# Kernel optimization log

Measured on AMD Instinct MI355X. Metric: run time of the kernel, lower is better.

## Reference

```python
import jax, jax.numpy as jnp
import numpy as np

WS = 8           # window_size
NH = 8           # num_heads
VD = 384         # values_dim
CD = 128         # coords_dim
ID = 384         # inner_dim = inner_ratio * values_dim
HD = ID // NH    # head_dim = 48


def _rel_bias(pos_emb):
    # static Swin relative-position index table, gathers from pos_emb [2*WS-1, 2*WS-1]
    idx = np.array([[x, y] for x in range(WS) for y in range(WS)])
    rel = idx[None, :, :] - idx[:, None, :] + WS - 1  # [64,64,2]
    return pos_emb[rel[:, :, 0], rel[:, :, 1]]        # [64,64]


def _rmsnorm(x, w, eps=1e-6):
    return x * jax.lax.rsqrt(jnp.mean(x * x, axis=-1, keepdims=True) + eps) * w


def _to_windows(t):
    # t: [b, Hp, Wp, D] with feature layout (e H) -> [b, NH, Wh, Ww, WS*WS, e]
    b, Hp, Wp, D = t.shape
    e = D // NH
    t = t.reshape(b, Hp // WS, WS, Wp // WS, WS, e, NH)
    t = t.transpose(0, 6, 1, 3, 2, 4, 5)
    return t.reshape(b, NH, Hp // WS, Wp // WS, WS * WS, e)


def setup_inputs() -> dict:
    key = jax.random.key(0)
    ks = jax.random.split(key, 8)
    B, H, W = 2, 192, 192
    s = 0.02
    return {
        "values": jax.random.normal(ks[0], (B, H, W, VD), jnp.float32),
        "coords": jax.random.normal(ks[1], (B, H, W, CD), jnp.float32),
        "W_vqk": jax.random.normal(ks[2], (VD, 2 * ID), jnp.float32) * s,
        "b_vqk": jnp.zeros((2 * ID,), jnp.float32),
        "g_vqk": jnp.ones((2 * ID,), jnp.float32),
        "W_vv": jax.random.normal(ks[3], (VD, ID), jnp.float32) * s,
        "b_vv": jnp.zeros((ID,), jnp.float32),
        "W_cqk": jax.random.normal(ks[4], (CD, 2 * ID), jnp.float32) * s,
        "b_cqk": jnp.zeros((2 * ID,), jnp.float32),
        "g_cqk": jnp.ones((2 * ID,), jnp.float32),
        "att_lambda": jax.random.normal(ks[5], (1,), jnp.float32),
        "pos_emb": jax.random.normal(ks[6], (2 * WS - 1, 2 * WS - 1), jnp.float32),
        "W_ov": jax.random.normal(ks[7], (ID, VD), jnp.float32) * s,
        "b_ov": jnp.zeros((VD,), jnp.float32),
    }


def reference(values, coords, W_vqk, b_vqk, g_vqk, W_vv, b_vv,
              W_cqk, b_cqk, g_cqk, att_lambda, pos_emb, W_ov, b_ov):
    b, h, w, _ = values.shape  # h, w divisible by WS -> torch F.pad would add 0
    # values path: cat([RMSNorm(Linear_qk(x)), Linear_v(x)]); '(d k)' with k=3
    # means q/k/v are INTERLEAVED along the feature dim (index d*3+k).
    vqk = _rmsnorm(values @ W_vqk + b_vqk, g_vqk)            # [b,h,w,2*ID]
    vv_ = values @ W_vv + b_vv                               # [b,h,w,ID]
    vcat = jnp.concatenate([vqk, vv_], axis=-1).reshape(b, h, w, ID, 3)
    qv, kv, vv = vcat[..., 0], vcat[..., 1], vcat[..., 2]
    # coords path (update_coords=False): interleaved split k=2
    cqk = _rmsnorm(coords @ W_cqk + b_cqk, g_cqk).reshape(b, h, w, ID, 2)
    qc, kc = cqk[..., 0], cqk[..., 1]
    # shifted=True: roll by -WS//2 (NOTE: original never rolls back)
    shift = -(WS // 2)
    roll = lambda t: jnp.roll(t, (shift, shift), axis=(1, 2))
    qv, kv, vv, qc, kc = (_to_windows(roll(t)) for t in (qv, kv, vv, qc, kc))
    # fused value+coord scores with learned lambda
    dots = (jnp.einsum('bHxyie,bHxyje->bHxyij', qv, kv)
            + att_lambda[0] * jnp.einsum('bHxyie,bHxyje->bHxyij', qc, kc)) / np.sqrt(HD)
    dots = dots + _rel_bias(pos_emb)
    # shifted-window masks on last window row / last window column
    s = WS * (WS // 2)
    n = WS * WS
    row_mask = jnp.zeros((n, n), jnp.float32)
    row_mask = row_mask.at[-s:, :-s].set(-jnp.inf).at[:-s, -s:].set(-jnp.inf)
    col_mask = row_mask.reshape(WS, WS, WS, WS).transpose(1, 0, 3, 2).reshape(n, n)
    dots = dots.at[:, :, -1, :].add(row_mask)
    dots = dots.at[:, :, :, -1].add(col_mask)
    att = jax.nn.softmax(dots, axis=-1)
    yv = jnp.einsum('bHxyij,bHxyje->bHxyie', att, vv)  # [b,NH,Wh,Ww,64,HD]
    Wh, Ww = h // WS, w // WS
    # output layout '(H e)' -> heads slow, e fast
    yv = yv.reshape(b, NH, Wh, Ww, WS, WS, HD).transpose(0, 2, 4, 3, 5, 1, 6)
    yv = yv.reshape(b, Wh * WS, Ww * WS, ID)[:, :h, :w, :]
    return yv @ W_ov + b_ov
```

## Files before the change

### kernel.cpp

```cpp
#include <hip/hip_runtime.h>
#include <hip/hip_bf16.h>

typedef __hip_bfloat16 bf16;
typedef __attribute__((ext_vector_type(8))) short bf16x8;
typedef __attribute__((ext_vector_type(4))) float f32x4;

#define CPIX 12288

__device__ __forceinline__ float tof(bf16 x){ return __bfloat162float(x); }
__device__ __forceinline__ bf16  tob(float x){ return __float2bfloat16(x); }
__device__ __forceinline__ float bf2f(short s){ return __uint_as_float(((unsigned)(unsigned short)s) << 16); }

__global__ __launch_bounds__(256) void wprep_k(
    const float* __restrict__ W_vqk, const float* __restrict__ W_vv, const float* __restrict__ W_cqk,
    const float* __restrict__ W_ov,  const float* __restrict__ b_vqk, const float* __restrict__ b_vv,
    const float* __restrict__ b_cqk, const float* __restrict__ g_vqk, const float* __restrict__ g_cqk,
    bf16* __restrict__ W1Tp, bf16* __restrict__ WcTp, bf16* __restrict__ WoT,
    float* __restrict__ bP0, float* __restrict__ bPc, float* __restrict__ gvP, float* __restrict__ gcP,
    float* __restrict__ rs_v, float* __restrict__ rs_c)
{
  int idx = blockIdx.x*256 + threadIdx.x;
  if (idx < 442368) {
    int n = idx/384, k = idx - n*384;
    int role = n/384, rem = n - role*384, h = rem/48, e = rem - (rem/48)*48;
    int c = 24*e + 3*h + role;
    float v = (e < 32) ? W_vqk[k*768 + c] : W_vv[k*384 + (c - 768)];
    W1Tp[n*384 + k] = tob(v);
  } else if (idx < 540672) {
    int q = idx - 442368;
    int n = q >> 7, k = q & 127;
    int role = n/384, rem = n - role*384, h = rem/48, e = rem - (rem/48)*48;
    WcTp[n*128 + k] = tob(W_cqk[k*768 + 16*e + 2*h + role]);
  } else if (idx < 688128) {
    int q = idx - 540672;
    int n = q/384, k = q - n*384;
    WoT[n*384 + k] = tob(W_ov[k*384 + n]);
  } else if (idx < 689280) {
    int n = idx - 688128;
    int role = n/384, rem = n - role*384, h = rem/48, e = rem - (rem/48)*48;
    int c = 24*e + 3*h + role;
    bP0[n] = (e < 32) ? b_vqk[c] : b_vv[c - 768];
  } else if (idx < 690048) {
    int n = idx - 689280;
    int role = n/384, rem = n - role*384, h = rem/48, e = rem - (rem/48)*48;
    bPc[n] = b_cqk[16*e + 2*h + role];
  } else if (idx < 691200) {
    int n = idx - 690048;
    int role = n/384, rem = n - role*384, h = rem/48, e = rem - (rem/48)*48;
    gvP[n] = (e < 32) ? g_vqk[24*e + 3*h + role] : 1.0f;
  } else if (idx < 691968) {
    int n = idx - 691200;
    int role = n/384, rem = n - role*384, h = rem/48, e = rem - (rem/48)*48;
    gcP[n] = g_cqk[16*e + 2*h + role];
  } else if (idx < 716544) {
    int q = idx - 691968;
    if (q < CPIX) rs_v[q] = 0.f; else rs_c[q - CPIX] = 0.f;
  }
}

template<int MODE>
__global__ __launch_bounds__(256,4) void gemm_k(const float* __restrict__ Af, const bf16* __restrict__ Ab,
    const bf16* __restrict__ WT, const float* __restrict__ biasP,
    bf16* __restrict__ outb, float* __restrict__ outf, float* __restrict__ rsum,
    float* __restrict__ z0, float* __restrict__ z1, int bb, int hf, int pix0)
{
  constexpr int KTOT = (MODE==1) ? 128 : 384;
  constexpr int NT   = (MODE==0) ? 1152 : (MODE==1) ? 768 : 384;
  constexpr int BM   = (MODE==2) ? 64 : 128;
  constexpr int MT4  = BM/32;
  constexpr int ACH  = BM*8;
  __shared__ bf16 As[BM][72];
  __shared__ bf16 Bs[128][72];
  const int tid = threadIdx.x, lane = tid & 63, wid = tid >> 6;
  const int wr = (wid >> 1)*(BM/2), wc = (wid & 1)*64;
  const int rowbase = blockIdx.x*BM;
  const int nbase   = blockIdx.y*128;

  if constexpr (MODE == 2) {
    if (blockIdx.y == 0) {
      if (tid < 64) z0[rowbase + tid] = 0.f;
      else if (tid < 128) z1[rowbase + tid - 64] = 0.f;
    }
  }

  f32x4 acc[MT4][4] = {};
  for (int ks = 0; ks < KTOT; ks += 64) {
    __syncthreads();
    #pragma unroll
    for (int it = 0; it < (ACH + 1024)/256; it++) {
      int idx = it*256 + tid;
      if (idx < ACH) {
        int r = idx >> 3, c = idx & 7;
        if constexpr (MODE == 2) {
          *(uint4*)&As[r][c*8] = *(const uint4*)(Ab + (size_t)(rowbase + r)*KTOT + ks + c*8);
        } else {
          int pix = rowbase + r;
          int lr = pix/192, lc = pix - (pix/192)*192;
          int srow = (hf*64 + lr + 4) % 192;
          int scol = (lc + 4) % 192;
          const float* src = Af + (((size_t)bb*192 + srow)*192 + scol)*KTOT + ks + c*8;
          float4 f0 = *(const float4*)src;
          float4 f1 = *(const float4*)(src + 4);
          union { bf16 h[8]; uint4 u4; } t;
          t.h[0]=tob(f0.x); t.h[1]=tob(f0.y); t.h[2]=tob(f0.z); t.h[3]=tob(f0.w);
          t.h[4]=tob(f1.x); t.h[5]=tob(f1.y); t.h[6]=tob(f1.z); t.h[7]=tob(f1.w);
          *(uint4*)&As[r][c*8] = t.u4;
        }
      } else {
        int q = idx - ACH; int r = q >> 3, c = q & 7;
        *(uint4*)&Bs[r][c*8] = *(const uint4*)(WT + (size_t)(nbase + r)*KTOT + ks + c*8);
      }
    }
    __syncthreads();
    #pragma unroll
    for (int k2 = 0; k2 < 64; k2 += 32) {
      const int kb = k2 + (lane >> 4)*8, ml = lane & 15;
      bf16x8 a[MT4], b[4];
      #pragma unroll
      for (int t = 0; t < MT4; t++) a[t] = *(const bf16x8*)&As[wr + t*16 + ml][kb];
      #pragma unroll
      for (int t = 0; t < 4; t++)  b[t] = *(const bf16x8*)&Bs[wc + t*16 + ml][kb];
      #pragma unroll
      for (int mt = 0; mt < MT4; mt++)
      #pragma unroll
      for (int nt = 0; nt < 4; nt++)
        acc[mt][nt] = __builtin_amdgcn_mfma_f32_16x16x32_bf16(a[mt], b[nt], acc[mt][nt], 0, 0, 0);
    }
  }
  const int lr4 = (lane >> 4)*4, lcol = lane & 15;
  #pragma unroll
  for (int mt = 0; mt < MT4; mt++) {
    #pragma unroll
    for (int i = 0; i < 4; i++) {
      int pix = rowbase + wr + mt*16 + lr4 + i;
      float sq_ = 0.f;
      #pragma unroll
      for (int nt = 0; nt < 4; nt++) {
        int n = nbase + wc + nt*16 + lcol;
        float v = acc[mt][nt][i] + biasP[n];
        if constexpr (MODE == 2) {
          outf[(size_t)(pix0 + pix)*384 + n] = v;
        } else {
          outb[(size_t)pix*NT + n] = tob(v);
          if (MODE == 1 || (n % 48) < 32) sq_ += v*v;
        }
      }
      if constexpr (MODE != 2) {
        sq_ += __shfl_xor(sq_, 1); sq_ += __shfl_xor(sq_, 2);
        sq_ += __shfl_xor(sq_, 4); sq_ += __shfl_xor(sq_, 8);
        if (lcol == 0) atomicAdd(&rsum[pix], sq_);
      }
    }
  }
}

__device__ __forceinline__ bf16x8 pack8g(uint4 raw, float r, float4 ga, float4 gb)
{
  union { uint4 u4; unsigned short us[8]; } rw; rw.u4 = raw;
  union { bf16x8 v; bf16 h[8]; } o;
  o.h[0] = tob(bf2f((short)rw.us[0]) * (r * ga.x));
  o.h[1] = tob(bf2f((short)rw.us[1]) * (r * ga.y));
  o.h[2] = tob(bf2f((short)rw.us[2]) * (r * ga.z));
  o.h[3] = tob(bf2f((short)rw.us[3]) * (r * ga.w));
  o.h[4] = tob(bf2f((short)rw.us[4]) * (r * gb.x));
  o.h[5] = tob(bf2f((short)rw.us[5]) * (r * gb.y));
  o.h[6] = tob(bf2f((short)rw.us[6]) * (r * gb.z));
  o.h[7] = tob(bf2f((short)rw.us[7]) * (r * gb.w));
  return o.v;
}

__device__ __forceinline__ float rmsf(float s){ return rsqrtf(s*(1.f/768.f) + 1e-6f); }

__global__ __launch_bounds__(256,4) void attn_k(const bf16* __restrict__ Y0, const bf16* __restrict__ Yc,
    const float* __restrict__ rs_v, const float* __restrict__ rs_c,
    const float* __restrict__ gvP, const float* __restrict__ gcP,
    const float* __restrict__ lam_p, const float* __restrict__ pos,
    bf16* __restrict__ y_att, int hf)
{
  __shared__ bf16 Ks[64][104];
  __shared__ bf16 Vt[48][72];
  __shared__ bf16 Pb[64][72];
  __shared__ float sq[96];
  __shared__ float poss[225];
  const int tid = threadIdx.x, lane = tid & 63, w = tid >> 6;
  const int win = blockIdx.x, h = blockIdx.y;
  const int wx = win/24, wy = win - (win/24)*24;
  const float lam = lam_p[0];
  const float SCL = 0.14433756729740643f;

  if (tid < 96) sq[tid] = (tid < 48 ? gvP[h*48 + tid] : gcP[h*48 + tid - 48]*lam) * SCL;
  if (tid < 225) poss[tid] = pos[tid];

  {
    const int j = lane;
    const int p = (wx*8 + (j>>3))*192 + wy*8 + (j&7);
    const float rvj = rmsf(rs_v[p]), rcj = rmsf(rs_c[p]);
    for (int grp = w; grp < 18; grp += 4) {
      if (grp < 6) {
        int c = grp;
        uint4 raw = *(const uint4*)(Y0 + (size_t)p*1152 + 384 + h*48 + c*8);
        const float* gp = gvP + 384 + h*48 + c*8;
        float4 ga = *(const float4*)gp, gb = *(const float4*)(gp+4);
        float r = (c < 4) ? rvj : 1.0f;
        union { bf16x8 v; uint4 u4; } o; o.v = pack8g(raw, r, ga, gb);
        *(uint4*)&Ks[j][c*8] = o.u4;
      } else if (grp < 12) {
        int c = grp - 6;
        uint4 raw = *(const uint4*)(Yc + (size_t)p*768 + 384 + h*48 + c*8);
        const float* gp = gcP + 384 + h*48 + c*8;
        float4 ga = *(const float4*)gp, gb = *(const float4*)(gp+4);
        union { bf16x8 v; uint4 u4; } o; o.v = pack8g(raw, rcj, ga, gb);
        *(uint4*)&Ks[j][48 + c*8] = o.u4;
      } else {
        int c = grp - 12;
        uint4 raw = *(const uint4*)(Y0 + (size_t)p*1152 + 768 + h*48 + c*8);
        const float* gp = gvP + 768 + h*48 + c*8;
        float4 ga = *(const float4*)gp, gb = *(const float4*)(gp+4);
        float r = (c < 4) ? rvj : 1.0f;
        union { uint4 u4; unsigned short us[8]; } rw; rw.u4 = raw;
        Vt[c*8+0][j] = tob(bf2f((short)rw.us[0]) * (r * ga.x));
        Vt[c*8+1][j] = tob(bf2f((short)rw.us[1]) * (r * ga.y));
        Vt[c*8+2][j] = tob(bf2f((short)rw.us[2]) * (r * ga.z));
        Vt[c*8+3][j] = tob(bf2f((short)rw.us[3]) * (r * ga.w));
        Vt[c*8+4][j] = tob(bf2f((short)rw.us[4]) * (r * gb.x));
        Vt[c*8+5][j] = tob(bf2f((short)rw.us[5]) * (r * gb.y));
        Vt[c*8+6][j] = tob(bf2f((short)rw.us[6]) * (r * gb.z));
        Vt[c*8+7][j] = tob(bf2f((short)rw.us[7]) * (r * gb.w));
      }
    }
  }
  __syncthreads();

  const int ml = lane & 15, k0 = (lane >> 4)*8;
  const int mrow = w*16 + ml;
  const int pA = (wx*8 + (mrow>>3))*192 + wy*8 + (mrow&7);
  const float rvA = rmsf(rs_v[pA]), rcA = rmsf(rs_c[pA]);
  bf16x8 qf0, qf1, qf2;
  {
    uint4 r0 = *(const uint4*)(Y0 + (size_t)pA*1152 + h*48 + k0);
    float4 ga = *(const float4*)&sq[k0],      gb = *(const float4*)&sq[k0+4];
    qf0 = pack8g(r0, rvA, ga, gb);
    const bf16* s1 = (k0 < 16) ? (Y0 + (size_t)pA*1152 + h*48 + 32 + k0)
                               : (Yc + (size_t)pA*768  + h*48 + (k0 - 16));
    float r1 = (k0 < 16) ? 1.0f : rcA;
    uint4 raw1 = *(const uint4*)s1;
    ga = *(const float4*)&sq[32+k0]; gb = *(const float4*)&sq[36+k0];
    qf1 = pack8g(raw1, r1, ga, gb);
    uint4 r2 = *(const uint4*)(Yc + (size_t)pA*768 + h*48 + 16 + k0);
    ga = *(const float4*)&sq[64+k0]; gb = *(const float4*)&sq[68+k0];
    qf2 = pack8g(r2, rcA, ga, gb);
  }

  f32x4 acc[4] = {};
  #pragma unroll
  for (int nt = 0; nt < 4; nt++) {
    bf16x8 b0 = *(const bf16x8*)&Ks[nt*16 + ml][k0];
    bf16x8 b1 = *(const bf16x8*)&Ks[nt*16 + ml][32 + k0];
    bf16x8 b2 = *(const bf16x8*)&Ks[nt*16 + ml][64 + k0];
    acc[nt] = __builtin_amdgcn_mfma_f32_16x16x32_bf16(qf0, b0, acc[nt], 0, 0, 0);
    acc[nt] = __builtin_amdgcn_mfma_f32_16x16x32_bf16(qf1, b1, acc[nt], 0, 0, 0);
    acc[nt] = __builtin_amdgcn_mfma_f32_16x16x32_bf16(qf2, b2, acc[nt], 0, 0, 0);
  }

  const bool rowm = (hf == 2) && (wx == 7);
  const bool colm = (wy == 23);
  const int g4 = (lane >> 4)*4;
  float pv[4][4];
  float inv_[4];
  #pragma unroll
  for (int i = 0; i < 4; i++) {
    int r = w*16 + g4 + i;
    int txi = r >> 3, tyi = r & 7;
    #pragma unroll
    for (int nt = 0; nt < 4; nt++) {
      int j = nt*16 + ml;
      int txj = j >> 3, tyj = j & 7;
      float v = acc[nt][i] + poss[(txj - txi + 7)*15 + (tyj - tyi + 7)];
      if ((rowm && ((txi >= 4) != (txj >= 4))) || (colm && ((tyi >= 4) != (tyj >= 4)))) v = -1e30f;
      pv[i][nt] = v;
    }
    float mx = fmaxf(fmaxf(pv[i][0], pv[i][1]), fmaxf(pv[i][2], pv[i][3]));
    #pragma unroll
    for (int m = 1; m < 16; m <<= 1) mx = fmaxf(mx, __shfl_xor(mx, m));
    float s0 = 0.f;
    #pragma unroll
    for (int nt = 0; nt < 4; nt++) { pv[i][nt] = __expf(pv[i][nt] - mx); s0 += pv[i][nt]; }
    #pragma unroll
    for (int m = 1; m < 16; m <<= 1) s0 += __shfl_xor(s0, m);
    inv_[i] = 1.f / s0;
  }
  #pragma unroll
  for (int i = 0; i < 4; i++)
  #pragma unroll
  for (int nt = 0; nt < 4; nt++)
    Pb[w*16 + g4 + i][nt*16 + ml] = tob(pv[i][nt]);

  f32x4 o0 = {}, o1 = {}, o2 = {};
  {
    bf16x8 a0 = *(const bf16x8*)&Pb[w*16 + ml][k0];
    bf16x8 b;
    b = *(const bf16x8*)&Vt[ 0 + ml][k0];      o0 = __builtin_amdgcn_mfma_f32_16x16x32_bf16(a0, b, o0, 0, 0, 0);
    b = *(const bf16x8*)&Vt[16 + ml][k0];      o1 = __builtin_amdgcn_mfma_f32_16x16x32_bf16(a0, b, o1, 0, 0, 0);
    b = *(const bf16x8*)&Vt[32 + ml][k0];      o2 = __builtin_amdgcn_mfma_f32_16x16x32_bf16(a0, b, o2, 0, 0, 0);
    bf16x8 a1 = *(const bf16x8*)&Pb[w*16 + ml][32 + k0];
    b = *(const bf16x8*)&Vt[ 0 + ml][32 + k0]; o0 = __builtin_amdgcn_mfma_f32_16x16x32_bf16(a1, b, o0, 0, 0, 0);
    b = *(const bf16x8*)&Vt[16 + ml][32 + k0]; o1 = __builtin_amdgcn_mfma_f32_16x16x32_bf16(a1, b, o1, 0, 0, 0);
    b = *(const bf16x8*)&Vt[32 + ml][32 + k0]; o2 = __builtin_amdgcn_mfma_f32_16x16x32_bf16(a1, b, o2, 0, 0, 0);
  }

  #pragma unroll
  for (int i = 0; i < 4; i++) {
    Pb[w*16 + g4 + i][     ml] = tob(o0[i] * inv_[i]);
    Pb[w*16 + g4 + i][16 + ml] = tob(o1[i] * inv_[i]);
    Pb[w*16 + g4 + i][32 + ml] = tob(o2[i] * inv_[i]);
  }
  #pragma unroll
  for (int s2 = 0; s2 < 3; s2++) {
    int u = s2*64 + lane;
    int row = u / 12, seg = u - row*12;
    int rr = w*16 + row;
    int pC = (wx*8 + (rr>>3))*192 + wy*8 + (rr&7);
    uint2 d = *(const uint2*)&Pb[rr][seg*4];
    *(uint2*)(y_att + (size_t)pC*384 + h*48 + seg*4) = d;
  }
}

extern "C" void kernel_launch(void* const* d_in, const int* in_sizes, int n_in,
                              void* d_out, int out_size, void* d_ws, size_t ws_size,
                              hipStream_t stream)
{
  const float* values = (const float*)d_in[0];
  const float* coords = (const float*)d_in[1];
  const float* W_vqk  = (const float*)d_in[2];
  const float* b_vqk  = (const float*)d_in[3];
  const float* g_vqk  = (const float*)d_in[4];
  const float* W_vv   = (const float*)d_in[5];
  const float* b_vv   = (const float*)d_in[6];
  const float* W_cqk  = (const float*)d_in[7];
  const float* b_cqk  = (const float*)d_in[8];
  const float* g_cqk  = (const float*)d_in[9];
  const float* lam    = (const float*)d_in[10];
  const float* pos    = (const float*)d_in[11];
  const float* W_ov   = (const float*)d_in[12];
  const float* b_ov   = (const float*)d_in[13];
  float* out = (float*)d_out;

  char* ws = (char*)d_ws;
  bf16*  W1Tp  = (bf16*)(ws + 0);
  bf16*  WcTp  = (bf16*)(ws + 884736);
  bf16*  WoT   = (bf16*)(ws + 1081344);
  float* bP0   = (float*)(ws + 1376256);
  float* bPc   = (float*)(ws + 1380864);
  float* gvP   = (float*)(ws + 1383936);
  float* gcP   = (float*)(ws + 1388544);
  bf16*  Y0    = (bf16*)(ws + 1391616);
  bf16*  Yc    = (bf16*)(ws + 29703168);
  float* rs_v  = (float*)(ws + 48577536);
  float* rs_c  = (float*)(ws + 48626688);
  bf16*  y_att = (bf16*)(ws + 48675840);
  (void)ws_size; (void)in_sizes; (void)n_in; (void)out_size;

  wprep_k<<<2799, 256, 0, stream>>>(W_vqk, W_vv, W_cqk, W_ov, b_vqk, b_vv, b_cqk, g_vqk, g_cqk,
                                    W1Tp, WcTp, WoT, bP0, bPc, gvP, gcP, rs_v, rs_c);

  for (int ch = 0; ch < 6; ch++) {
    int bb = ch/3, hf = ch - bb*3;
    gemm_k<0><<<dim3(96,9), 256, 0, stream>>>(values, nullptr, W1Tp, bP0, Y0, nullptr, rs_v,
                                              nullptr, nullptr, bb, hf, 0);
    gemm_k<1><<<dim3(96,6), 256, 0, stream>>>(coords, nullptr, WcTp, bPc, Yc, nullptr, rs_c,
                                              nullptr, nullptr, bb, hf, 0);
    attn_k<<<dim3(192,8), 256, 0, stream>>>(Y0, Yc, rs_v, rs_c, gvP, gcP, lam, pos, y_att, hf);
    gemm_k<2><<<dim3(192,3), 256, 0, stream>>>(nullptr, y_att, WoT, b_ov, nullptr, out, nullptr,
                                               rs_v, rs_c, 0, 0, ch*CPIX);
  }
}
```

Measured before the change: 696.9 us.

## Merge value/coord projection GEMMs and prefetch next K-tile into registers

Combines the value and coord QK projection GEMMs into one launch, with blockIdx.y selecting the path, so both fill the GPU together and one launch is saved per chunk. Both this GEMM and the output GEMM now register-prefetch the next K slice while MFMAs run on the current LDS tile, hiding global load latency. The attention kernel occupancy hint goes from 4 to 5 blocks per CU. Register prefetching raises register pressure, and the projection GEMM's occupancy hint drops to 3.

```diff
diff --git a/kernel.cpp b/kernel.cpp
--- a/kernel.cpp
+++ b/kernel.cpp
@@ -58,78 +58,91 @@
   }
 }
 
-template<int MODE>
-__global__ __launch_bounds__(256,4) void gemm_k(const float* __restrict__ Af, const bf16* __restrict__ Ab,
-    const bf16* __restrict__ WT, const float* __restrict__ biasP,
-    bf16* __restrict__ outb, float* __restrict__ outf, float* __restrict__ rsum,
-    float* __restrict__ z0, float* __restrict__ z1, int bb, int hf, int pix0)
-{
-  constexpr int KTOT = (MODE==1) ? 128 : 384;
-  constexpr int NT   = (MODE==0) ? 1152 : (MODE==1) ? 768 : 384;
-  constexpr int BM   = (MODE==2) ? 64 : 128;
-  constexpr int MT4  = BM/32;
-  constexpr int ACH  = BM*8;
-  __shared__ bf16 As[BM][72];
+__global__ __launch_bounds__(256,3) void gemmqk_k(
+    const float* __restrict__ Vf, const float* __restrict__ Cf,
+    const bf16* __restrict__ W1Tp, const bf16* __restrict__ WcTp,
+    const float* __restrict__ bP0, const float* __restrict__ bPc,
+    bf16* __restrict__ Y0, bf16* __restrict__ Yc,
+    float* __restrict__ rs_v, float* __restrict__ rs_c,
+    int bb, int hf)
+{
+  const bool isc = (blockIdx.y >= 9);
+  const int KTOT = isc ? 128 : 384;
+  const int NT   = isc ? 768 : 1152;
+  const float* Af = isc ? Cf : Vf;
+  const bf16*  WT = isc ? WcTp : W1Tp;
+  const float* biasP = isc ? bPc : bP0;
+  bf16* outb  = isc ? Yc : Y0;
+  float* rsum = isc ? rs_c : rs_v;
+  const int nbase   = (isc ? (blockIdx.y - 9) : blockIdx.y)*128;
+  const int rowbase = blockIdx.x*128;
+
+  __shared__ bf16 As[128][72];
   __shared__ bf16 Bs[128][72];
   const int tid = threadIdx.x, lane = tid & 63, wid = tid >> 6;
-  const int wr = (wid >> 1)*(BM/2), wc = (wid & 1)*64;
-  const int rowbase = blockIdx.x*BM;
-  const int nbase   = blockIdx.y*128;
-
-  if constexpr (MODE == 2) {
-    if (blockIdx.y == 0) {
-      if (tid < 64) z0[rowbase + tid] = 0.f;
-      else if (tid < 128) z1[rowbase + tid - 64] = 0.f;
-    }
-  }
-
-  f32x4 acc[MT4][4] = {};
+  const int wr = (wid >> 1)*64, wc = (wid & 1)*64;
+
+  unsigned abase[4];
+  #pragma unroll
+  for (int it = 0; it < 4; it++) {
+    int idx = it*256 + tid, r = idx >> 3, c = idx & 7;
+    int pix = rowbase + r;
+    int lr = pix/192, lc = pix - (pix/192)*192;
+    int srow = (hf*64 + lr + 4) % 192;
+    int scol = (lc + 4) % 192;
+    abase[it] = (unsigned)(((bb*192 + srow)*192 + scol)*KTOT + c*8);
+  }
+
+  float4 pa[4][2];
+  uint4  pb[4];
+
+  #pragma unroll
+  for (int it = 0; it < 4; it++) {
+    const float* s = Af + abase[it];
+    pa[it][0] = *(const float4*)s;  pa[it][1] = *(const float4*)(s + 4);
+    int idx = it*256 + tid, r = idx >> 3, c = idx & 7;
+    pb[it] = *(const uint4*)(WT + (size_t)(nbase + r)*KTOT + c*8);
+  }
+
+  f32x4 acc[4][4] = {};
   for (int ks = 0; ks < KTOT; ks += 64) {
+    #pragma unroll
+    for (int it = 0; it < 4; it++) {
+      int idx = it*256 + tid, r = idx >> 3, c = idx & 7;
+      union { bf16 h[8]; uint4 u4; } t;
+      t.h[0]=tob(pa[it][0].x); t.h[1]=tob(pa[it][0].y); t.h[2]=tob(pa[it][0].z); t.h[3]=tob(pa[it][0].w);
+      t.h[4]=tob(pa[it][1].x); t.h[5]=tob(pa[it][1].y); t.h[6]=tob(pa[it][1].z); t.h[7]=tob(pa[it][1].w);
+      *(uint4*)&As[r][c*8] = t.u4;
+      *(uint4*)&Bs[r][c*8] = pb[it];
+    }
     __syncthreads();
-    #pragma unroll
-    for (int it = 0; it < (ACH + 1024)/256; it++) {
-      int idx = it*256 + tid;
-      if (idx < ACH) {
-        int r = idx >> 3, c = idx & 7;
-        if constexpr (MODE == 2) {
-          *(uint4*)&As[r][c*8] = *(const uint4*)(Ab + (size_t)(rowbase + r)*KTOT + ks + c*8);
-        } else {
-          int pix = rowbase + r;
-          int lr = pix/192, lc = pix - (pix/192)*192;
-          int srow = (hf*64 + lr + 4) % 192;
-          int scol = (lc + 4) % 192;
-          const float* src = Af + (((size_t)bb*192 + srow)*192 + scol)*KTOT + ks + c*8;
-          float4 f0 = *(const float4*)src;
-          float4 f1 = *(const float4*)(src + 4);
-          union { bf16 h[8]; uint4 u4; } t;
-          t.h[0]=tob(f0.x); t.h[1]=tob(f0.y); t.h[2]=tob(f0.z); t.h[3]=tob(f0.w);
-          t.h[4]=tob(f1.x); t.h[5]=tob(f1.y); t.h[6]=tob(f1.z); t.h[7]=tob(f1.w);
-          *(uint4*)&As[r][c*8] = t.u4;
-        }
-      } else {
-        int q = idx - ACH; int r = q >> 3, c = q & 7;
-        *(uint4*)&Bs[r][c*8] = *(const uint4*)(WT + (size_t)(nbase + r)*KTOT + ks + c*8);
+    if (ks + 64 < KTOT) {
+      #pragma unroll
+      for (int it = 0; it < 4; it++) {
+        const float* s = Af + abase[it] + (ks + 64);
+        pa[it][0] = *(const float4*)s;  pa[it][1] = *(const float4*)(s + 4);
+        int idx = it*256 + tid, r = idx >> 3, c = idx & 7;
+        pb[it] = *(const uint4*)(WT + (size_t)(nbase + r)*KTOT + (ks + 64) + c*8);
       }
     }
-    __syncthreads();
     #pragma unroll
     for (int k2 = 0; k2 < 64; k2 += 32) {
       const int kb = k2 + (lane >> 4)*8, ml = lane & 15;
-      bf16x8 a[MT4], b[4];
-      #pragma unroll
-      for (int t = 0; t < MT4; t++) a[t] = *(const bf16x8*)&As[wr + t*16 + ml][kb];
-      #pragma unroll
-      for (int t = 0; t < 4; t++)  b[t] = *(const bf16x8*)&Bs[wc + t*16 + ml][kb];
-      #pragma unroll
-      for (int mt = 0; mt < MT4; mt++)
+      bf16x8 a[4], b[4];
+      #pragma unroll
+      for (int t = 0; t < 4; t++) { a[t] = *(const bf16x8*)&As[wr + t*16 + ml][kb];
+                                    b[t] = *(const bf16x8*)&Bs[wc + t*16 + ml][kb]; }
+      #pragma unroll
+      for (int mt = 0; mt < 4; mt++)
       #pragma unroll
       for (int nt = 0; nt < 4; nt++)
         acc[mt][nt] = __builtin_amdgcn_mfma_f32_16x16x32_bf16(a[mt], b[nt], acc[mt][nt], 0, 0, 0);
     }
+    __syncthreads();
   }
   const int lr4 = (lane >> 4)*4, lcol = lane & 15;
   #pragma unroll
-  for (int mt = 0; mt < MT4; mt++) {
+  for (int mt = 0; mt < 4; mt++) {
     #pragma unroll
     for (int i = 0; i < 4; i++) {
       int pix = rowbase + wr + mt*16 + lr4 + i;
@@ -138,18 +151,97 @@
       for (int nt = 0; nt < 4; nt++) {
         int n = nbase + wc + nt*16 + lcol;
         float v = acc[mt][nt][i] + biasP[n];
-        if constexpr (MODE == 2) {
-          outf[(size_t)(pix0 + pix)*384 + n] = v;
-        } else {
-          outb[(size_t)pix*NT + n] = tob(v);
-          if (MODE == 1 || (n % 48) < 32) sq_ += v*v;
-        }
+        outb[(size_t)pix*NT + n] = tob(v);
+        if (isc || (n % 48) < 32) sq_ += v*v;
       }
-      if constexpr (MODE != 2) {
-        sq_ += __shfl_xor(sq_, 1); sq_ += __shfl_xor(sq_, 2);
-        sq_ += __shfl_xor(sq_, 4); sq_ += __shfl_xor(sq_, 8);
-        if (lcol == 0) atomicAdd(&rsum[pix], sq_);
+      sq_ += __shfl_xor(sq_, 1); sq_ += __shfl_xor(sq_, 2);
+      sq_ += __shfl_xor(sq_, 4); sq_ += __shfl_xor(sq_, 8);
+      if (lcol == 0) atomicAdd(&rsum[pix], sq_);
+    }
+  }
+}
+
+__global__ __launch_bounds__(256,4) void gemmo_k(const bf16* __restrict__ Ab, const bf16* __restrict__ WT,
+    const float* __restrict__ biasP, float* __restrict__ outf,
+    float* __restrict__ z0, float* __restrict__ z1, int pix0)
+{
+  __shared__ bf16 As[64][72];
+  __shared__ bf16 Bs[128][72];
+  const int tid = threadIdx.x, lane = tid & 63, wid = tid >> 6;
+  const int wr = (wid >> 1)*32, wc = (wid & 1)*64;
+  const int rowbase = blockIdx.x*64;
+  const int nbase   = blockIdx.y*128;
+
+  if (blockIdx.y == 0) {
+    if (tid < 64) z0[rowbase + tid] = 0.f;
+    else if (tid < 128) z1[rowbase + tid - 64] = 0.f;
+  }
+
+  uint4 pa[2], pb[4];
+  #pragma unroll
+  for (int it = 0; it < 2; it++) {
+    int idx = it*256 + tid, r = idx >> 3, c = idx & 7;
+    pa[it] = *(const uint4*)(Ab + (size_t)(rowbase + r)*384 + c*8);
+  }
+  #pragma unroll
+  for (int it = 0; it < 4; it++) {
+    int idx = it*256 + tid, r = idx >> 3, c = idx & 7;
+    pb[it] = *(const uint4*)(WT + (size_t)(nbase + r)*384 + c*8);
+  }
+
+  f32x4 acc[2][4] = {};
+  for (int ks = 0; ks < 384; ks += 64) {
+    #pragma unroll
+    for (int it = 0; it < 2; it++) {
+      int idx = it*256 + tid, r = idx >> 3, c = idx & 7;
+      *(uint4*)&As[r][c*8] = pa[it];
+    }
+    #pragma unroll
+    for (int it = 0; it < 4; it++) {
+      int idx = it*256 + tid, r = idx >> 3, c = idx & 7;
+      *(uint4*)&Bs[r][c*8] = pb[it];
+    }
+    __syncthreads();
+    if (ks + 64 < 384) {
+      #pragma unroll
+      for (int it = 0; it < 2; it++) {
+        int idx = it*256 + tid, r = idx >> 3, c = idx & 7;
+        pa[it] = *(const uint4*)(Ab + (size_t)(rowbase + r)*384 + (ks + 64) + c*8);
       }
+      #pragma unroll
+      for (int it = 0; it < 4; it++) {
+        int idx = it*256 + tid, r = idx >> 3, c = idx & 7;
+        pb[it] = *(const uint4*)(WT + (size_t)(nbase + r)*384 + (ks + 64) + c*8);
+      }
+    }
+    #pragma unroll
+    for (int k2 = 0; k2 < 64; k2 += 32) {
+      const int kb = k2 + (lane >> 4)*8, ml = lane & 15;
+      bf16x8 a[2], b[4];
+      #pragma unroll
+      for (int t = 0; t < 2; t++) a[t] = *(const bf16x8*)&As[wr + t*16 + ml][kb];
+      #pragma unroll
+      for (int t = 0; t < 4; t++) b[t] = *(const bf16x8*)&Bs[wc + t*16 + ml][kb];
+      #pragma unroll
+      for (int mt = 0; mt < 2; mt++)
+      #pragma unroll
+      for (int nt = 0; nt < 4; nt++)
+        acc[mt][nt] = __builtin_amdgcn_mfma_f32_16x16x32_bf16(a[mt], b[nt], acc[mt][nt], 0, 0, 0);
+    }
+    __syncthreads();
+  }
+  const int lr4 = (lane >> 4)*4, lcol = lane & 15;
+  #pragma unroll
+  for (int mt = 0; mt < 2; mt++)
+  #pragma unroll
+  for (int nt = 0; nt < 4; nt++) {
+    f32x4 av = acc[mt][nt];
+    int n = nbase + wc + nt*16 + lcol;
+    float bv = biasP[n];
+    #pragma unroll
+    for (int i = 0; i < 4; i++) {
+      int pix = rowbase + wr + mt*16 + lr4 + i;
+      outf[(size_t)(pix0 + pix)*384 + n] = av[i] + bv;
     }
   }
 }
@@ -171,7 +263,7 @@
 
 __device__ __forceinline__ float rmsf(float s){ return rsqrtf(s*(1.f/768.f) + 1e-6f); }
 
-__global__ __launch_bounds__(256,4) void attn_k(const bf16* __restrict__ Y0, const bf16* __restrict__ Yc,
+__global__ __launch_bounds__(256,5) void attn_k(const bf16* __restrict__ Y0, const bf16* __restrict__ Yc,
     const float* __restrict__ rs_v, const float* __restrict__ rs_c,
     const float* __restrict__ gvP, const float* __restrict__ gcP,
     const float* __restrict__ lam_p, const float* __restrict__ pos,
@@ -365,12 +457,9 @@
 
   for (int ch = 0; ch < 6; ch++) {
     int bb = ch/3, hf = ch - bb*3;
-    gemm_k<0><<<dim3(96,9), 256, 0, stream>>>(values, nullptr, W1Tp, bP0, Y0, nullptr, rs_v,
-                                              nullptr, nullptr, bb, hf, 0);
-    gemm_k<1><<<dim3(96,6), 256, 0, stream>>>(coords, nullptr, WcTp, bPc, Yc, nullptr, rs_c,
-                                              nullptr, nullptr, bb, hf, 0);
+    gemmqk_k<<<dim3(96,15), 256, 0, stream>>>(values, coords, W1Tp, WcTp, bP0, bPc,
+                                              Y0, Yc, rs_v, rs_c, bb, hf);
     attn_k<<<dim3(192,8), 256, 0, stream>>>(Y0, Yc, rs_v, rs_c, gvP, gcP, lam, pos, y_att, hf);
-    gemm_k<2><<<dim3(192,3), 256, 0, stream>>>(nullptr, y_att, WoT, b_ov, nullptr, out, nullptr,
-                                               rs_v, rs_c, 0, 0, ch*CPIX);
-  }
-}
+    gemmo_k<<<dim3(192,3), 256, 0, stream>>>(y_att, WoT, b_ov, out, rs_v, rs_c, ch*CPIX);
+  }
+}
```

New measurement: 859.6 us. +23.3%, slower.
